# Kernel tuning notes

Measured on AMD Instinct MI355X. Metric: run time of the kernel, lower is better.

Reference implementation:

```python
import jax, jax.numpy as jnp
import numpy as np

B, N, F_IN, H_DIM, HEADS, DH, LAYERS, OUT, BS = 8192, 64, 12, 64, 4, 16, 3, 128, 8
LN_EPS = 1e-5


def _build_adj():
    # 8-neighbor grid adjacency + self loops, as in _register_adjacency
    adj = np.zeros((N, N), np.float32)
    for i in range(N):
        r, c = divmod(i, BS)
        for dr in (-1, 0, 1):
            for dc in (-1, 0, 1):
                if dr == 0 and dc == 0:
                    continue
            
                nr, nc = r + dr, c + dc
                if 0 <= nr < BS and 0 <= nc < BS:
                    adj[i, nr * BS + nc] = 1.0
    adj += np.eye(N, dtype=np.float32)
    return (adj > 0).astype(np.int32)


def setup_inputs() -> dict:
    key = jax.random.key(0)
    ks = jax.random.split(key, 16)
    s = 0.05
    return {
        "x": jax.random.normal(ks[0], (B, N, F_IN), jnp.float32),
        "adj": jnp.asarray(_build_adj()),
        "W_in": jax.random.normal(ks[1], (F_IN, H_DIM), jnp.float32) * s,
        "b_in": jnp.zeros((H_DIM,), jnp.float32),
        "Wq": jax.random.normal(ks[2], (LAYERS, H_DIM, H_DIM), jnp.float32) * s,
        "Wk": jax.random.normal(ks[3], (LAYERS, H_DIM, H_DIM), jnp.float32) * s,
        "Wv": jax.random.normal(ks[4], (LAYERS, H_DIM, H_DIM), jnp.float32) * s,
        "Wo": jax.random.normal(ks[5], (LAYERS, H_DIM, H_DIM), jnp.float32) * s,
        "bo": jnp.zeros((LAYERS, H_DIM), jnp.float32),
        "ln_g": jnp.ones((LAYERS, H_DIM), jnp.float32),
        "ln_b": jnp.zeros((LAYERS, H_DIM), jnp.float32),
        "Wp1": jax.random.normal(ks[6], (H_DIM, H_DIM), jnp.float32) * s,
        "bp1": jnp.zeros((H_DIM,), jnp.float32),
        "Wp2": jax.random.normal(ks[7], (H_DIM, OUT), jnp.float32) * s,
        "bp2": jnp.zeros((OUT,), jnp.float32),
    }


def _layer_norm(h, g, b):
    mu = jnp.mean(h, axis=-1, keepdims=True)
    var = jnp.mean(jnp.square(h - mu), axis=-1, keepdims=True)
    return (h - mu) * jax.lax.rsqrt(var + LN_EPS) * g + b


def reference(x, adj, W_in, b_in, Wq, Wk, Wv, Wo, bo, ln_g, ln_b, Wp1, bp1, Wp2, bp2):
    b, n = x.shape[:2]
    mask = (adj == 0)[None, None]          # (1,1,N,N)
    scale = 1.0 / jnp.sqrt(jnp.float32(DH))
    h = x @ W_in + b_in                    # (B,N,H_DIM)
    for l in range(LAYERS):
        q = (h @ Wq[l]).reshape(b, n, HEADS, DH)
        k = (h @ Wk[l]).reshape(b, n, HEADS, DH)
        v = (h @ Wv[l]).reshape(b, n, HEADS, DH)
        scores = jnp.einsum('bihd,bjhd->bhij', q, k) * scale   # (B,H,N,N)
        scores = jnp.where(mask, -jnp.inf, scores)
        attn = jax.nn.softmax(scores, axis=-1)                 # dropout = identity (eval)
        o = jnp.einsum('bhij,bjhd->bihd', attn, v).reshape(b, n, HEADS * DH)
        o = o @ Wo[l] + bo[l]
        h = _layer_norm(h + o, ln_g[l], ln_b[l])
    pooled = h.mean(axis=1)                                    # (B,H_DIM)
    return jax.nn.relu(pooled @ Wp1 + bp1) @ Wp2 + bp2         # (B,OUT)
```

## Files before the change

### kernel.cpp

```cpp
#include <hip/hip_runtime.h>
#include <stdint.h>

#define NB       64
#define FIN      12
#define HD       64
#define NHEADS   4
#define DHEAD    16
#define NLAYERS  3
#define ODIM     128
#define LN_EPS   1e-5f
#define BTOT     8192

#define NTH      256
#define NW       (NLAYERS * 4)
#define WFRAG    4096
#define WIN_U16  2048
#define NTILES   10
#define MSK_U32  (NTILES * 64 * 2)

#define STR      20
#define HSTR     (64 * STR)

typedef unsigned int       u32;
typedef unsigned short     u16;
typedef unsigned long long u64;
typedef _Float16           f16;

typedef f16    f16x8 __attribute__((ext_vector_type(8)));
typedef f16    f16x4 __attribute__((ext_vector_type(4)));
typedef f16    h2    __attribute__((ext_vector_type(2)));
typedef __fp16 hh2   __attribute__((ext_vector_type(2)));
typedef float  f32x4 __attribute__((ext_vector_type(4)));
union U128h { uint4 u; f16x8 v8; h2 v2[4]; };
union U64h  { uint2 u; f16x4 v4; h2 h[2]; u32 w[2]; u16 s[4]; };

#if __has_builtin(__builtin_amdgcn_exp2f)
  __device__ __forceinline__ float e2(float x) { return __builtin_amdgcn_exp2f(x); }
#else
  __device__ __forceinline__ float e2(float x) { return exp2f(x); }
#endif

__device__ __forceinline__ float fdot2h(h2 a, h2 b, float c) {
#if __has_builtin(__builtin_amdgcn_fdot2)
  return __builtin_amdgcn_fdot2(a, b, c, false);
#else
  return c + (float)a[0] * (float)b[0] + (float)a[1] * (float)b[1];
#endif
}

#if __has_builtin(__builtin_amdgcn_cvt_pkrtz)
__device__ __forceinline__ u32 packh2(float a, float b) {
  hh2 p = __builtin_amdgcn_cvt_pkrtz(a, b);
  return *(u32*)&p;
}
#else
__device__ __forceinline__ u32 packh2(float a, float b) {
  h2 p = {(f16)a, (f16)b};
  return *(u32*)&p;
}
#endif
__device__ __forceinline__ void wb4(u16* __restrict__ dst, f32x4 a) {
  *(uint2*)dst = make_uint2(packh2(a[0], a[1]), packh2(a[2], a[3]));
}

#if __has_builtin(__builtin_amdgcn_mfma_f32_16x16x16f16)
__device__ __forceinline__ f32x4 mfma16(f16x4 a, f16x4 b, f32x4 c) {
  return __builtin_amdgcn_mfma_f32_16x16x16f16(a, b, c, 0, 0, 0);
}
#elif __has_builtin(__builtin_amdgcn_mfma_f32_16x16x16_f16)
__device__ __forceinline__ f32x4 mfma16(f16x4 a, f16x4 b, f32x4 c) {
  return __builtin_amdgcn_mfma_f32_16x16x16_f16(a, b, c, 0, 0, 0);
}
#else
__device__ __forceinline__ f32x4 mfma16(f16x4 a, f16x4 b, f32x4 c) {
  f16x8 a8 = {a[0], a[1], a[2], a[3], (f16)0, (f16)0, (f16)0, (f16)0};
  f16x8 b8 = {b[0], b[1], b[2], b[3], (f16)0, (f16)0, (f16)0, (f16)0};
  return __builtin_amdgcn_mfma_f32_16x16x32_f16(a8, b8, c, 0, 0, 0);
}
#endif

struct __align__(16) Smem {
  u16 Qh[NHEADS * HSTR];
  u16 Kh[NHEADS * HSTR];
  u16 Vh[NHEADS * HSTR];
  u32 Msk[MSK_U32];
};

extern "C" __global__ void __launch_bounds__(256)
prep_pack(const float* __restrict__ Wq, const float* __restrict__ Wk,
          const float* __restrict__ Wv, const float* __restrict__ Wo,
          const float* __restrict__ W_in, const int* __restrict__ adj,
          u16* __restrict__ wsW) {
  const int w = blockIdx.x;
  if (w < NW) {
    const int l = w >> 2, ty = w & 3;
    const float* src = (ty == 0 ? Wq : ty == 1 ? Wk : ty == 2 ? Wv : Wo) + l * HD * HD;
    const float sc = (ty == 0) ? (0.25f * 1.44269504f) : 1.0f;
    u16* dst = wsW + w * WFRAG;
    for (int f = threadIdx.x; f < 512; f += 256) {
      const int lane = f & 63, kh = (f >> 6) & 1, nt = f >> 7;
      const int n  = nt * 16 + (lane & 15);
      const int k0 = kh * 32 + ((lane >> 4) & 3) * 8;
      u16 tmp[8];
      #pragma unroll
      for (int j = 0; j < 8; ++j) {
        f16 hv = (f16)(src[(k0 + j) * HD + n] * sc);
        tmp[j] = *(u16*)&hv;
      }
      *(uint4*)(dst + f * 8) = *(const uint4*)tmp;
    }
  } else if (w == NW) {
    const int t = threadIdx.x;
    const int mt = t >> 6, lane = t & 63;
    const int mm = lane & 15, qq = (lane >> 4) & 3;
    u16 tmp[8];
    #pragma unroll
    for (int j = 0; j < 8; ++j) {
      const int k = qq * 8 + j;
      f16 hv = (k < FIN) ? (f16)W_in[k * HD + mt * 16 + mm] : (f16)0.0f;
      tmp[j] = *(u16*)&hv;
    }
    *(uint4*)(wsW + NW * WFRAG + t * 8) = *(const uint4*)tmp;
  } else {
    static const int TIv[NTILES] = {0, 0, 1, 1, 1, 2, 2, 2, 3, 3};
    static const int TJv[NTILES] = {0, 1, 0, 1, 2, 1, 2, 3, 2, 3};
    u32* wsMsk = (u32*)(wsW + NW * WFRAG + WIN_U16);
    for (int idx = threadIdx.x; idx < MSK_U32; idx += 256) {
      const int tile = idx >> 7, rem = idx & 127;
      const int l = rem >> 1, pr = rem & 1;
      const int i  = TIv[tile] * 16 + (l & 15);
      const int j0 = TJv[tile] * 16 + ((l >> 4) & 3) * 4 + pr * 2;
      const u32 lo = (adj[i * NB + j0]     != 0) ? 0x3C00u : 0u;
      const u32 hi = (adj[i * NB + j0 + 1] != 0) ? 0x3C00u : 0u;
      wsMsk[idx] = lo | (hi << 16);
    }
  }
}

__device__ __forceinline__ void mmT(const u16* __restrict__ wf, U128h b0, U128h b1,
                                    int lane, f32x4 acc[4]) {
  #pragma unroll
  for (int mt = 0; mt < 4; ++mt) {
    U128h a0, a1;
    a0.u = *(const uint4*)(wf + ((mt * 2 + 0) * 64 + lane) * 8);
    a1.u = *(const uint4*)(wf + ((mt * 2 + 1) * 64 + lane) * 8);
    acc[mt] = __builtin_amdgcn_mfma_f32_16x16x32_f16(a0.v8, b0.v8, acc[mt], 0, 0, 0);
    acc[mt] = __builtin_amdgcn_mfma_f32_16x16x32_f16(a1.v8, b1.v8, acc[mt], 0, 0, 0);
  }
}

__device__ __forceinline__ void make_bfrags(const float hr[4][4], int q, int m,
                                            U128h& b0, U128h& b1) {
  u32 p[8];
  #pragma unroll
  for (int mt = 0; mt < 4; ++mt) {
    p[2 * mt]     = packh2(hr[mt][0], hr[mt][1]);
    p[2 * mt + 1] = packh2(hr[mt][2], hr[mt][3]);
  }
  const int sA = (2 * (q & 1)) * 16 + m;
  const int sB = sA + 16;
  u32 A[8], B[8];
  #pragma unroll
  for (int k = 0; k < 8; ++k) A[k] = (u32)__shfl((int)p[k], sA, 64);
  #pragma unroll
  for (int k = 0; k < 8; ++k) B[k] = (u32)__shfl((int)p[k], sB, 64);
  const bool hi = (q & 2) != 0;
  b0.u.x = hi ? A[2] : A[0];  b0.u.y = hi ? A[3] : A[1];
  b0.u.z = hi ? B[2] : B[0];  b0.u.w = hi ? B[3] : B[1];
  b1.u.x = hi ? A[6] : A[4];  b1.u.y = hi ? A[7] : A[5];
  b1.u.z = hi ? B[6] : B[4];  b1.u.w = hi ? B[7] : B[5];
}

extern "C" __global__ void __launch_bounds__(NTH, 4)
gnn_fused(const float* __restrict__ x, const float* __restrict__ b_in,
          const u16* __restrict__ wsW, const float* __restrict__ bo,
          const float* __restrict__ ln_g, const float* __restrict__ ln_b,
          const float* __restrict__ Wp1, const float* __restrict__ bp1,
          const float* __restrict__ Wp2, const float* __restrict__ bp2,
          float* __restrict__ out) {
  __shared__ Smem s;
  const int t    = threadIdx.x;
  const int lane = t & 63;
  const int wv   = t >> 6;
  const int eg   = (int)blockIdx.x;
  const int m    = lane & 15, q = lane >> 4;
  const int node = wv * 16 + m;

  const u16* wsWin = wsW + NW * WFRAG;

  ((uint4*)s.Kh)[t] = make_uint4(0u, 0u, 0u, 0u);
  {
    const uint4* mg4 = (const uint4*)(wsWin + WIN_U16);
    ((uint4*)s.Msk)[t] = mg4[t];
    if (t < 64) ((uint4*)s.Msk)[256 + t] = mg4[256 + t];
  }
  __syncthreads();
  if (t < (NB * FIN) / 4) {
    const int nd = t / 3, pos = (t % 3) * 4;
    const float4 v4 = *(const float4*)(x + eg * NB * FIN + t * 4);
    *(uint2*)&s.Kh[nd * 32 + pos] = make_uint2(packh2(v4.x, v4.y), packh2(v4.z, v4.w));
  }
  __syncthreads();

  float hr[4][4];
  {
    U128h xb;
    xb.u = *(const uint4*)&s.Kh[node * 32 + q * 8];
    #pragma unroll
    for (int mt = 0; mt < 4; ++mt) {
      U128h a0;
      a0.u = *(const uint4*)(wsWin + (mt * 64 + lane) * 8);
      f32x4 acc = {0.f, 0.f, 0.f, 0.f};
      acc = __builtin_amdgcn_mfma_f32_16x16x32_f16(a0.v8, xb.v8, acc, 0, 0, 0);
      const f32x4 b4 = *(const f32x4*)&b_in[mt * 16 + q * 4];
      #pragma unroll
      for (int r = 0; r < 4; ++r) hr[mt][r] = acc[r] + b4[r];
    }
  }
  __syncthreads();

  for (int l = 0; l < NLAYERS; ++l) {
    const u16* wl = wsW + (l * 4) * WFRAG;

    {
      U128h b0, b1;
      make_bfrags(hr, q, m, b0, b1);

      f32x4 aq[4] = {{0,0,0,0},{0,0,0,0},{0,0,0,0},{0,0,0,0}};
      mmT(wl + 0 * WFRAG, b0, b1, lane, aq);
      #pragma unroll
      for (int mt = 0; mt < 4; ++mt)
        wb4(&s.Qh[mt * HSTR + node * STR + q * 4], aq[mt]);

      f32x4 ak[4] = {{0,0,0,0},{0,0,0,0},{0,0,0,0},{0,0,0,0}};
      mmT(wl + 1 * WFRAG, b0, b1, lane, ak);
      #pragma unroll
      for (int mt = 0; mt < 4; ++mt)
        wb4(&s.Kh[mt * HSTR + node * STR + q * 4], ak[mt]);

      f32x4 av[4] = {{0,0,0,0},{0,0,0,0},{0,0,0,0},{0,0,0,0}};
      mmT(wl + 2 * WFRAG, b0, b1, lane, av);
      #pragma unroll
      for (int mt = 0; mt < 4; ++mt)
        wb4(&s.Vh[mt * HSTR + node * STR + q * 4], av[mt]);
    }
    __syncthreads();

    {
      const int hh = wv;
      const u16* Qp = s.Qh + hh * HSTR;
      const u16* Kp = s.Kh + hh * HSTR;
      const u16* Vp = s.Vh + hh * HSTR;
      u16*       Op = s.Qh + hh * HSTR;
      const h2 one2 = {(f16)1.0f, (f16)1.0f};
      const f32x4 z4 = {0.f, 0.f, 0.f, 0.f};

      f16x4 kf[4], vf[4];
      #pragma unroll
      for (int tj = 0; tj < 4; ++tj) {
        U64h tk; tk.u = *(const uint2*)&Kp[(tj * 16 + m) * STR + q * 4];
        kf[tj] = tk.v4;
      }
      #pragma unroll
      for (int kt = 0; kt < 4; ++kt) {
        const int j0 = kt * 16 + q * 4;
        U64h tv;
        tv.s[0] = Vp[(j0 + 0) * STR + m];
        tv.s[1] = Vp[(j0 + 1) * STR + m];
        tv.s[2] = Vp[(j0 + 2) * STR + m];
        tv.s[3] = Vp[(j0 + 3) * STR + m];
        vf[kt] = tv.v4;
      }

#define ATTN_TI(TI, TJ0, NTJ, T0)                                              \
      {                                                                        \
        U64h tq; tq.u = *(const uint2*)&Qp[((TI) * 16 + m) * STR + q * 4];     \
        const f16x4 qf = tq.v4;                                                \
        f32x4 ot = z4;                                                         \
        float dsum = 0.0f;                                                     \
        _Pragma("unroll")                                                      \
        for (int dt = 0; dt < (NTJ); ++dt) {                                   \
          const int tj = (TJ0) + dt;                                           \
          f32x4 st = mfma16(kf[tj], qf, z4);                                   \
          const uint2 mmv = *(const uint2*)&s.Msk[((T0) + dt) * 128 + (lane << 1)]; \
          U64h pp;                                                             \
          pp.w[0] = packh2(e2(st[0]), e2(st[1]));                              \
          pp.w[1] = packh2(e2(st[2]), e2(st[3]));                              \
          pp.h[0] *= *(const h2*)&mmv.x;                                       \
          pp.h[1] *= *(const h2*)&mmv.y;                                       \
          dsum = fdot2h(pp.h[0], one2, dsum);                                  \
          dsum = fdot2h(pp.h[1], one2, dsum);                                  \
          ot = mfma16(vf[tj], pp.v4, ot);                                      \
        }                                                                      \
        dsum += __shfl_xor(dsum, 16, 64);                                      \
        dsum += __shfl_xor(dsum, 32, 64);                                      \
        const float rinv = 1.0f / dsum;                                        \
        ot[0] *= rinv; ot[1] *= rinv; ot[2] *= rinv; ot[3] *= rinv;            \
        wb4(&Op[((TI) * 16 + m) * STR + q * 4], ot);                           \
      }

      ATTN_TI(0, 0, 2, 0)
      ATTN_TI(1, 0, 3, 2)
      ATTN_TI(2, 1, 3, 5)
      ATTN_TI(3, 2, 2, 8)
#undef ATTN_TI
    }
    __syncthreads();

    {
      const int hq = q >> 1, dof = (q & 1) * 8;
      const u16* ob0 = &s.Qh[hq * HSTR + node * STR + dof];
      const u16* ob1 = &s.Qh[(2 + hq) * HSTR + node * STR + dof];
      U128h b0, b1;
      const uint2 x0 = *(const uint2*)ob0, x1 = *(const uint2*)(ob0 + 4);
      const uint2 y0 = *(const uint2*)ob1, y1v = *(const uint2*)(ob1 + 4);
      b0.u = make_uint4(x0.x, x0.y, x1.x, x1.y);
      b1.u = make_uint4(y0.x, y0.y, y1v.x, y1v.y);
      f32x4 ao[4] = {{0,0,0,0},{0,0,0,0},{0,0,0,0},{0,0,0,0}};
      mmT(wl + 3 * WFRAG, b0, b1, lane, ao);

      float uu[4][4];
      float s1 = 0.0f, s2 = 0.0f;
      #pragma unroll
      for (int mt = 0; mt < 4; ++mt) {
        const f32x4 bo4 = *(const f32x4*)&bo[l * HD + mt * 16 + q * 4];
        #pragma unroll
        for (int r = 0; r < 4; ++r) {
          const float v = hr[mt][r] + ao[mt][r] + bo4[r];
          uu[mt][r] = v;
          s1 += v;
          s2 += v * v;
        }
      }
      s1 += __shfl_xor(s1, 16, 64); s1 += __shfl_xor(s1, 32, 64);
      s2 += __shfl_xor(s2, 16, 64); s2 += __shfl_xor(s2, 32, 64);
      const float mu  = s1 * (1.0f / 64.0f);
      const float var = s2 * (1.0f / 64.0f) - mu * mu;
      const float rs  = rsqrtf(var + LN_EPS);
      #pragma unroll
      for (int mt = 0; mt < 4; ++mt) {
        const f32x4 g4 = *(const f32x4*)&ln_g[l * HD + mt * 16 + q * 4];
        const f32x4 b4 = *(const f32x4*)&ln_b[l * HD + mt * 16 + q * 4];
        #pragma unroll
        for (int r = 0; r < 4; ++r)
          hr[mt][r] = (uu[mt][r] - mu) * rs * g4[r] + b4[r];
      }
    }
    if (l + 1 < NLAYERS) __syncthreads();
  }

  float* pool = (float*)s.Kh;
  float* y1   = pool + HD;
  __syncthreads();
  if (t < HD) pool[t] = 0.0f;
  __syncthreads();
  {
    #pragma unroll
    for (int mt = 0; mt < 4; ++mt)
      #pragma unroll
      for (int r = 0; r < 4; ++r) {
        float v = hr[mt][r];
        v += __shfl_xor(v, 1, 64); v += __shfl_xor(v, 2, 64);
        v += __shfl_xor(v, 4, 64); v += __shfl_xor(v, 8, 64);
        hr[mt][r] = v;
      }
    if (m == 0) {
      #pragma unroll
      for (int mt = 0; mt < 4; ++mt)
        #pragma unroll
        for (int r = 0; r < 4; ++r)
          atomicAdd(&pool[mt * 16 + q * 4 + r], hr[mt][r] * (1.0f / 64.0f));
    }
  }
  __syncthreads();
  if (t < HD) {
    float acc = bp1[t];
    #pragma unroll 8
    for (int k = 0; k < HD; ++k) acc = fmaf(pool[k], Wp1[k * HD + t], acc);
    y1[t] = fmaxf(acc, 0.0f);
  }
  __syncthreads();
  if (t < ODIM) {
    float acc = bp2[t];
    #pragma unroll 8
    for (int c = 0; c < HD; ++c) acc = fmaf(y1[c], Wp2[c * ODIM + t], acc);
    out[eg * ODIM + t] = acc;
  }
}

extern "C" void kernel_launch(void* const* d_in, const int* in_sizes, int n_in,
                              void* d_out, int out_size, void* d_ws, size_t ws_size,
                              hipStream_t stream) {
  const float* x    = (const float*)d_in[0];
  const int*   adj  = (const int*)d_in[1];
  const float* W_in = (const float*)d_in[2];
  const float* b_in = (const float*)d_in[3];
  const float* Wq   = (const float*)d_in[4];
  const float* Wk   = (const float*)d_in[5];
  const float* Wv   = (const float*)d_in[6];
  const float* Wo   = (const float*)d_in[7];
  const float* bo   = (const float*)d_in[8];
  const float* lng  = (const float*)d_in[9];
  const float* lnb  = (const float*)d_in[10];
  const float* Wp1  = (const float*)d_in[11];
  const float* bp1  = (const float*)d_in[12];
  const float* Wp2  = (const float*)d_in[13];
  const float* bp2  = (const float*)d_in[14];
  float* outp = (float*)d_out;
  u16*   wsW  = (u16*)d_ws;

  hipLaunchKernelGGL(prep_pack, dim3(NW + 2), dim3(256), 0, stream,
                     Wq, Wk, Wv, Wo, W_in, adj, wsW);
  hipLaunchKernelGGL(gnn_fused, dim3(BTOT), dim3(NTH), 0, stream,
                     x, b_in, wsW, bo, lng, lnb, Wp1, bp1, Wp2, bp2, outp);
}
```

Before: 283.4 us.

## Stage weight fragments into double-buffered LDS via async global-to-LDS loads

Each Q/K/V/O weight fragment is copied into a two-slot LDS buffer with global_load_lds. The next fragment is prefetched while the current one is consumed by the MFMAs, and the next layer's Wq is prefetched during the output projection. The aim is to replace repeated per-wave global/L2 reads of the weights with shared-memory reads and to hide the load latency. In exchange it adds two block barriers per layer and 16 KB of LDS per block, and lowers the launch-bounds occupancy hint from 4 to 3 blocks.

```diff
diff --git a/kernel.cpp b/kernel.cpp
--- a/kernel.cpp
+++ b/kernel.cpp
@@ -84,6 +84,7 @@
   u16 Kh[NHEADS * HSTR];
   u16 Vh[NHEADS * HSTR];
   u32 Msk[MSK_U32];
+  u16 Wbuf[2][WFRAG];
 };
 
 extern "C" __global__ void __launch_bounds__(256)
@@ -137,7 +138,27 @@
   }
 }
 
-__device__ __forceinline__ void mmT(const u16* __restrict__ wf, U128h b0, U128h b1,
+__device__ __forceinline__ void stageW(const u16* __restrict__ src, u16* dst,
+                                       int wv, int lane) {
+#if __has_builtin(__builtin_amdgcn_global_load_lds)
+  #pragma unroll
+  for (int r = 0; r < 2; ++r) {
+    const u16* g = src + (r * 4 + wv) * 512 + lane * 8;
+    u16* d = dst + (r * 4 + wv) * 512;
+    __builtin_amdgcn_global_load_lds(
+        (const __attribute__((address_space(1))) void*)g,
+        (__attribute__((address_space(3))) void*)d, 16, 0, 0);
+  }
+#else
+  #pragma unroll
+  for (int r = 0; r < 2; ++r) {
+    const uint4 v = *(const uint4*)(src + (r * 4 + wv) * 512 + lane * 8);
+    *(uint4*)(dst + (r * 4 + wv) * 512 + lane * 8) = v;
+  }
+#endif
+}
+
+__device__ __forceinline__ void mmT(const u16* wf, U128h b0, U128h b1,
                                     int lane, f32x4 acc[4]) {
   #pragma unroll
   for (int mt = 0; mt < 4; ++mt) {
@@ -171,7 +192,7 @@
   b1.u.z = hi ? B[6] : B[4];  b1.u.w = hi ? B[7] : B[5];
 }
 
-extern "C" __global__ void __launch_bounds__(NTH, 4)
+extern "C" __global__ void __launch_bounds__(NTH, 3)
 gnn_fused(const float* __restrict__ x, const float* __restrict__ b_in,
           const u16* __restrict__ wsW, const float* __restrict__ bo,
           const float* __restrict__ ln_g, const float* __restrict__ ln_b,
@@ -200,6 +221,7 @@
     const float4 v4 = *(const float4*)(x + eg * NB * FIN + t * 4);
     *(uint2*)&s.Kh[nd * 32 + pos] = make_uint2(packh2(v4.x, v4.y), packh2(v4.z, v4.w));
   }
+  stageW(wsW + 0 * WFRAG, s.Wbuf[0], wv, lane);
   __syncthreads();
 
   float hr[4][4];
@@ -226,20 +248,25 @@
       U128h b0, b1;
       make_bfrags(hr, q, m, b0, b1);
 
+      stageW(wl + 1 * WFRAG, s.Wbuf[1], wv, lane);
       f32x4 aq[4] = {{0,0,0,0},{0,0,0,0},{0,0,0,0},{0,0,0,0}};
-      mmT(wl + 0 * WFRAG, b0, b1, lane, aq);
+      mmT(s.Wbuf[0], b0, b1, lane, aq);
       #pragma unroll
       for (int mt = 0; mt < 4; ++mt)
         wb4(&s.Qh[mt * HSTR + node * STR + q * 4], aq[mt]);
-
+      __syncthreads();
+
+      stageW(wl + 2 * WFRAG, s.Wbuf[0], wv, lane);
       f32x4 ak[4] = {{0,0,0,0},{0,0,0,0},{0,0,0,0},{0,0,0,0}};
-      mmT(wl + 1 * WFRAG, b0, b1, lane, ak);
+      mmT(s.Wbuf[1], b0, b1, lane, ak);
       #pragma unroll
       for (int mt = 0; mt < 4; ++mt)
         wb4(&s.Kh[mt * HSTR + node * STR + q * 4], ak[mt]);
-
+      __syncthreads();
+
+      stageW(wl + 3 * WFRAG, s.Wbuf[1], wv, lane);
       f32x4 av[4] = {{0,0,0,0},{0,0,0,0},{0,0,0,0},{0,0,0,0}};
-      mmT(wl + 2 * WFRAG, b0, b1, lane, av);
+      mmT(s.Wbuf[0], b0, b1, lane, av);
       #pragma unroll
       for (int mt = 0; mt < 4; ++mt)
         wb4(&s.Vh[mt * HSTR + node * STR + q * 4], av[mt]);
@@ -308,6 +335,9 @@
     __syncthreads();
 
     {
+      if (l + 1 < NLAYERS)
+        stageW(wsW + ((l + 1) * 4) * WFRAG, s.Wbuf[0], wv, lane);
+
       const int hq = q >> 1, dof = (q & 1) * 8;
       const u16* ob0 = &s.Qh[hq * HSTR + node * STR + dof];
       const u16* ob1 = &s.Qh[(2 + hq) * HSTR + node * STR + dof];
@@ -317,7 +347,7 @@
       b0.u = make_uint4(x0.x, x0.y, x1.x, x1.y);
       b1.u = make_uint4(y0.x, y0.y, y1v.x, y1v.y);
       f32x4 ao[4] = {{0,0,0,0},{0,0,0,0},{0,0,0,0},{0,0,0,0}};
-      mmT(wl + 3 * WFRAG, b0, b1, lane, ao);
+      mmT(s.Wbuf[1], b0, b1, lane, ao);
 
       float uu[4][4];
       float s1 = 0.0f, s2 = 0.0f;
```

Result: slower. 294.0 us (+3.7%).
